# Performance work log

Hardware: AMD Instinct MI355X
Metric: run time of the kernel (lower is better)

Reference implementation:

```python
import jax, jax.numpy as jnp
from jax import lax
import numpy as np

_MAX_SQRT_GRADIENT = 1000.0

@jax.custom_vjp
def sqrt_bound_derivative(x):
    return jnp.sqrt(x)

def _sbd_fwd(x):
    return jnp.sqrt(x), x

def _sbd_bwd(x, g):
    clipped = jnp.clip(4.0 * x, 1.0 / _MAX_SQRT_GRADIENT**2)
    return (g / jnp.sqrt(clipped),)

sqrt_bound_derivative.defvjp(_sbd_fwd, _sbd_bwd)

HIDDEN = 2560
LRU = 2560
HEADS = 10
CONV_W = 4
BATCH = 2
SEQ = 4096


def setup_inputs() -> dict:
    key = jax.random.key(0)
    ks = jax.random.split(key, 12)
    s = 0.02  # init scale for weights
    inp = {
        'input_states': jax.random.normal(ks[0], (BATCH, SEQ, HIDDEN), jnp.float32),
        'position_ids': jnp.broadcast_to(jnp.arange(SEQ, dtype=jnp.int64), (BATCH, SEQ)),
        'prev_h': jnp.zeros((BATCH, LRU), jnp.float32),
        'w_y': jax.random.normal(ks[1], (LRU, HIDDEN), jnp.float32) * s,
        'b_y': jax.random.normal(ks[2], (LRU,), jnp.float32) * s,
        'w_x': jax.random.normal(ks[3], (LRU, HIDDEN), jnp.float32) * s,
        'b_x': jax.random.normal(ks[4], (LRU,), jnp.float32) * s,
        'w_out': jax.random.normal(ks[5], (HIDDEN, LRU), jnp.float32) * s,
        'b_out': jax.random.normal(ks[6], (HIDDEN,), jnp.float32) * s,
        'conv_w': jax.random.normal(ks[7], (LRU, CONV_W), jnp.float32) * 0.3,
        'conv_b': jax.random.normal(ks[8], (LRU,), jnp.float32) * s,
        'a_param': jax.random.normal(ks[9], (LRU,), jnp.float32),
        'ig_w': jax.random.normal(ks[10], (LRU // HEADS, LRU), jnp.float32) * s,
        'ig_b': jnp.zeros((LRU // HEADS,), jnp.float32),
        'ag_w': jax.random.normal(ks[11], (LRU // HEADS, LRU), jnp.float32) * s,
        'ag_b': jnp.zeros((LRU // HEADS,), jnp.float32),
    }
    return inp


def _block_gate(x_bshi, gate_w, gate_b, heads, bw):
    # gate_w is the nn.Linear weight [bw, heads*bw] reshaped to block-diagonal form
    w = gate_w.reshape(heads, bw, bw).transpose(0, 2, 1)  # h i j
    y = jnp.einsum('bshi,hij->bshj', x_bshi, w) + gate_b
    B, S = y.shape[0], y.shape[1]
    return jax.nn.sigmoid(y.reshape(B, S, heads * bw))


def _rglru(activations, position_ids, prev_h, a_param, ig_w, ig_b, ag_w, ag_b):
    B, S, D = activations.shape
    bw = ig_w.shape[0]
    heads = ig_w.shape[1] // bw
    reset = (position_ids[:, :, None] == 0)  # [B,S,1] bool
    x = activations.reshape(B, S, heads, bw)
    gate_x = _block_gate(x, ig_w, ig_b, heads, bw)  # [B,S,D]
    gate_a = _block_gate(x, ag_w, ag_b, heads, bw)  # [B,S,D]
    log_a = -8.0 * gate_a * jax.nn.softplus(a_param)
    a = jnp.exp(log_a)
    a_square = jnp.exp(2.0 * log_a)
    gated_x = activations * gate_x
    multiplier = sqrt_bound_derivative(1.0 - a_square)
    multiplier = jnp.where(reset, 1.0, multiplier)
    normalized_x = gated_x * multiplier.astype(activations.dtype)
    a = a * (~reset)  # zero the decay at document boundaries

    def step(h, inp):
        a_t, x_t = inp  # [B,D] each
        h = a_t.astype(jnp.float32) * h + x_t.astype(jnp.float32)
        return h, h.astype(activations.dtype)

    xs = (a.transpose(1, 0, 2), normalized_x.transpose(1, 0, 2))  # time-major
    last_h, y = lax.scan(step, prev_h, xs)
    return y.transpose(1, 0, 2), last_h


def reference(input_states, position_ids, prev_h, w_y, b_y, w_x, b_x,
              w_out, b_out, conv_w, conv_b, a_param, ig_w, ig_b, ag_w, ag_b):
    B, S, _ = input_states.shape
    # y branch: gelu(tanh approx)
    y_branch = jax.nn.gelu(input_states @ w_y.T + b_y, approximate=True)
    # x branch: linear + depthwise causal conv (kernel width CONV_W)
    x_branch = input_states @ w_x.T + b_x  # [B,S,LRU]
    Wd = conv_w.shape[1]
    xp = jnp.pad(x_branch, ((0, 0), (Wd - 1, 0), (0, 0)))
    conv_out = conv_b + sum(xp[:, k:k + S, :] * conv_w[:, k] for k in range(Wd))
    # RG-LRU
    h, last_h = _rglru(conv_out, position_ids, prev_h, a_param, ig_w, ig_b, ag_w, ag_b)
    h = h * y_branch
    out = h @ w_out.T + b_out
    return out
```

## Files before the change

### kernel.cpp

```cpp
#include <hip/hip_runtime.h>
#include <hip/hip_bf16.h>
#include <math.h>

typedef __hip_bfloat16 bf16;
typedef __attribute__((ext_vector_type(4))) float f32x4;
typedef __attribute__((ext_vector_type(8))) __bf16 bf16x8;

static constexpr int HID    = 2560;
static constexpr int LRUD   = 2560;
static constexpr int HEADSN = 10;
static constexpr int BWID   = 256;
static constexpr int SEQL   = 4096;
static constexpr int BATCHN = 2;
static constexpr int NTOK   = BATCHN * SEQL;
static constexpr int NCHUNK = 128;
static constexpr int CHLEN  = 32;

#define GAS __attribute__((address_space(1)))
#define LAS __attribute__((address_space(3)))
#define MEMFENCE asm volatile("" ::: "memory")
#define PHASE_SYNC                                        \
  __builtin_amdgcn_s_barrier(); MEMFENCE;                 \
  asm volatile("s_waitcnt lgkmcnt(0)" ::: "memory");
#define PHASE_END                                         \
  __builtin_amdgcn_s_barrier(); MEMFENCE;
#define VMGATE6 asm volatile("s_waitcnt vmcnt(6)" ::: "memory")
#define VMGATE0 asm volatile("s_waitcnt vmcnt(0)" ::: "memory")

__device__ __forceinline__ void async_copy16(void* lds, const void* g) {
  __builtin_amdgcn_global_load_lds((const GAS unsigned int*)g,
                                   (LAS unsigned int*)lds, 16, 0, 0);
}

__device__ __forceinline__ bf16x8 lds_frag(const bf16* tile, int row, int cb) {
  return *(const bf16x8*)((const char*)tile + row * 128 + (cb ^ ((row & 7) << 4)));
}

template<int EPI>
__global__ __launch_bounds__(512, 2)
void gemm256_kernel(const bf16* __restrict__ A, int lda,
                    const bf16* __restrict__ B0p, const bf16* __restrict__ B1p,
                    int ldb,
                    const float* __restrict__ bias0, const float* __restrict__ bias1,
                    void* __restrict__ out0, void* __restrict__ out1,
                    int ldc, int K)
{
  __shared__ __align__(16) bf16 As[2][256 * 64];
  __shared__ __align__(16) bf16 Bs[2][256 * 64];

  const int tid  = threadIdx.x;
  const int wave = tid >> 6;
  const int lane = tid & 63;
  const int wm   = wave >> 2;
  const int wn   = wave & 3;

  const int nxy  = gridDim.x * gridDim.y;
  const int orig = blockIdx.y * gridDim.x + blockIdx.x;
  const int swz  = (orig & 7) * (nxy >> 3) + (orig >> 3);
  const int m0   = (swz / gridDim.x) * 256;
  const int n0   = (swz % gridDim.x) * 256;

  const int zsel = (EPI == 1) ? (int)blockIdx.z : 0;
  const bf16*  Bw   = zsel ? B1p : B0p;
  const float* bias = zsel ? bias1 : bias0;

  const int NT = K / 64;
  f32x4  acc[8][4] = {};
  bf16x8 a[8], b[4][2];

  const int srow = tid >> 3;
  const int spb  = (tid & 7) * 16;

  auto stageA = [&](int t, int c) {
    const int r  = c * 64 + srow;
    const int cb = spb ^ ((r & 7) << 4);
    async_copy16(&As[t & 1][c * 4096 + wave * 512],
                 A + (size_t)(m0 + r) * lda + t * 64 + (cb >> 1));
  };
  auto stageB = [&](int t, int c) {
    const int r  = c * 64 + srow;
    const int cb = spb ^ ((r & 7) << 4);
    async_copy16(&Bs[t & 1][c * 4096 + wave * 512],
                 Bw + (size_t)(n0 + r) * ldb + t * 64 + (cb >> 1));
  };
  auto readA = [&](int buf, int ks) {
#pragma unroll
    for (int fm = 0; fm < 8; ++fm)
      a[fm] = lds_frag(As[buf], wm * 128 + fm * 16 + (lane & 15),
                       ks * 64 + (lane >> 4) * 16);
  };
  auto readB = [&](int buf) {
#pragma unroll
    for (int fn = 0; fn < 4; ++fn)
#pragma unroll
      for (int ks = 0; ks < 2; ++ks)
        b[fn][ks] = lds_frag(Bs[buf], wn * 64 + fn * 16 + (lane & 15),
                             ks * 64 + (lane >> 4) * 16);
  };
  auto mfma16 = [&](int ks, int fnb) {
#pragma unroll
    for (int fn = 0; fn < 4; ++fn) {
      if (fn != fnb && fn != fnb + 1) continue;
#pragma unroll
      for (int fm = 0; fm < 8; ++fm)
        acc[fm][fn] = __builtin_amdgcn_mfma_f32_16x16x32_bf16(a[fm], b[fn][ks],
                                                              acc[fm][fn], 0, 0, 0);
    }
  };

#pragma unroll
  for (int c = 0; c < 4; ++c) stageA(0, c);
#pragma unroll
  for (int c = 0; c < 4; ++c) stageB(0, c);
#pragma unroll
  for (int c = 0; c < 4; ++c) stageB(1, c);
  stageA(1, 0); stageA(1, 1);
  VMGATE6;
  PHASE_END;

  const int NI = NT / 2;
  for (int i = 0; i < NI; ++i) {
    const int  t0 = 2 * i, t1 = 2 * i + 1;
    const bool s2 = (t0 + 2) < NT;
    const bool s3 = (t1 + 2) < NT;

    readA(0, 0); readB(0);
    stageA(t1, 2); stageA(t1, 3);
    PHASE_SYNC;
    __builtin_amdgcn_s_setprio(1); mfma16(0, 0); __builtin_amdgcn_s_setprio(0);
    PHASE_END;
    if (s2) { stageB(t0 + 2, 0); stageB(t0 + 2, 1); }
    PHASE_SYNC;
    __builtin_amdgcn_s_setprio(1); mfma16(0, 2); __builtin_amdgcn_s_setprio(0);
    PHASE_END;
    readA(0, 1);
    if (s2) { stageB(t0 + 2, 2); stageB(t0 + 2, 3); }
    PHASE_SYNC;
    __builtin_amdgcn_s_setprio(1); mfma16(1, 0); __builtin_amdgcn_s_setprio(0);
    PHASE_END;
    if (s2) { stageA(t0 + 2, 0); stageA(t0 + 2, 1); }
    PHASE_SYNC;
    __builtin_amdgcn_s_setprio(1); mfma16(1, 2); __builtin_amdgcn_s_setprio(0);
    if (s2) { VMGATE6; } else { VMGATE0; }
    PHASE_END;
    readA(1, 0); readB(1);
    if (s2) { stageA(t0 + 2, 2); stageA(t0 + 2, 3); }
    PHASE_SYNC;
    __builtin_amdgcn_s_setprio(1); mfma16(0, 0); __builtin_amdgcn_s_setprio(0);
    PHASE_END;
    if (s3) { stageB(t1 + 2, 0); stageB(t1 + 2, 1); }
    PHASE_SYNC;
    __builtin_amdgcn_s_setprio(1); mfma16(0, 2); __builtin_amdgcn_s_setprio(0);
    PHASE_END;
    readA(1, 1);
    if (s3) { stageB(t1 + 2, 2); stageB(t1 + 2, 3); }
    PHASE_SYNC;
    __builtin_amdgcn_s_setprio(1); mfma16(1, 0); __builtin_amdgcn_s_setprio(0);
    PHASE_END;
    if (s3) { stageA(t1 + 2, 0); stageA(t1 + 2, 1); }
    PHASE_SYNC;
    __builtin_amdgcn_s_setprio(1); mfma16(1, 2); __builtin_amdgcn_s_setprio(0);
    if (s2) { if (s3) { VMGATE6; } else { VMGATE0; } }
    PHASE_END;
  }

  const int mrb = (lane >> 4) * 4;
  const int ncc = lane & 15;
#pragma unroll
  for (int fm = 0; fm < 8; ++fm) {
#pragma unroll
    for (int fn = 0; fn < 4; ++fn) {
      const int n  = n0 + wn * 64 + fn * 16 + ncc;
      const float bv = bias[n];
#pragma unroll
      for (int r = 0; r < 4; ++r) {
        const int m = m0 + wm * 128 + fm * 16 + mrb + r;
        const size_t idx = (size_t)m * ldc + n;
        float v = acc[fm][fn][r] + bv;
        if constexpr (EPI == 0) {
          ((float*)out0)[idx] = v;
        } else {
          if (zsel == 0) {
            const float t = tanhf(0.7978845608028654f * (v + 0.044715f * v * v * v));
            ((bf16*)out0)[idx] = __float2bfloat16(0.5f * v * (1.0f + t));
          } else {
            ((bf16*)out1)[idx] = __float2bfloat16(v);
          }
        }
      }
    }
  }
}

__global__ __launch_bounds__(256)
void gemm128_f32_kernel(const bf16* __restrict__ A, int lda,
                        const bf16* __restrict__ Bw, int ldb,
                        const float* __restrict__ bias,
                        float* __restrict__ C, int ldc, int K)
{
  __shared__ __align__(16) bf16 As[128 * 64];
  __shared__ __align__(16) bf16 Bs[128 * 64];

  const int tid  = threadIdx.x;
  const int wave = tid >> 6;
  const int lane = tid & 63;
  const int wy   = wave >> 1;
  const int wx   = wave & 1;
  const int m0   = blockIdx.y * 128;
  const int n0   = blockIdx.x * 128;

  f32x4 acc[4][4] = {};
  const int srow = tid >> 3;
  const int spb  = (tid & 7) * 16;

  for (int k0 = 0; k0 < K; k0 += 64) {
#pragma unroll
    for (int rd = 0; rd < 4; ++rd) {
      const int r  = rd * 32 + srow;
      const int cb = spb ^ ((r & 7) << 4);
      async_copy16(&As[rd * 2048 + wave * 512],
                   A + (size_t)(m0 + r) * lda + k0 + (cb >> 1));
      async_copy16(&Bs[rd * 2048 + wave * 512],
                   Bw + (size_t)(n0 + r) * ldb + k0 + (cb >> 1));
    }
    __syncthreads();
#pragma unroll
    for (int ks = 0; ks < 2; ++ks) {
      bf16x8 af[4], bfr[4];
      const int cb = ks * 64 + (lane >> 4) * 16;
#pragma unroll
      for (int f = 0; f < 4; ++f) {
        af[f]  = lds_frag(As, wy * 64 + f * 16 + (lane & 15), cb);
        bfr[f] = lds_frag(Bs, wx * 64 + f * 16 + (lane & 15), cb);
      }
#pragma unroll
      for (int fm = 0; fm < 4; ++fm)
#pragma unroll
        for (int fn = 0; fn < 4; ++fn)
          acc[fm][fn] = __builtin_amdgcn_mfma_f32_16x16x32_bf16(af[fm], bfr[fn], acc[fm][fn], 0, 0, 0);
    }
    __syncthreads();
  }

  const int mrb = (lane >> 4) * 4;
  const int ncc = lane & 15;
#pragma unroll
  for (int fm = 0; fm < 4; ++fm) {
#pragma unroll
    for (int fn = 0; fn < 4; ++fn) {
      const int n  = n0 + wx * 64 + fn * 16 + ncc;
      const float bv = bias[n];
#pragma unroll
      for (int r = 0; r < 4; ++r) {
        const int m = m0 + wy * 64 + fm * 16 + mrb + r;
        C[(size_t)m * ldc + n] = acc[fm][fn][r] + bv;
      }
    }
  }
}

__global__ __launch_bounds__(256)
void gate_gemm_kernel(const bf16* __restrict__ Conv,
                      const bf16* __restrict__ IGb, const bf16* __restrict__ AGb,
                      const float* __restrict__ ig_b, const float* __restrict__ ag_b,
                      bf16* __restrict__ Gx, bf16* __restrict__ Ga)
{
  __shared__ __align__(16) bf16 As[128 * 64];
  __shared__ __align__(16) bf16 Bs[128 * 64];

  const int tid  = threadIdx.x;
  const int wave = tid >> 6;
  const int lane = tid & 63;
  const int wy   = wave >> 1;
  const int wx   = wave & 1;
  const int m0   = blockIdx.y * 128;
  const int n0   = blockIdx.x * 128;
  const int head = blockIdx.z % HEADSN;
  const int sel  = blockIdx.z / HEADSN;

  const bf16*  A    = Conv + head * BWID;
  const bf16*  Bw   = (sel ? AGb : IGb) + (size_t)head * BWID * BWID;
  const float* bias = sel ? ag_b : ig_b;
  bf16*        Cp   = (sel ? Ga : Gx) + head * BWID;

  f32x4 acc[4][4] = {};
  const int srow = tid >> 3;
  const int spb  = (tid & 7) * 16;

  for (int k0 = 0; k0 < BWID; k0 += 64) {
#pragma unroll
    for (int rd = 0; rd < 4; ++rd) {
      const int r  = rd * 32 + srow;
      const int cb = spb ^ ((r & 7) << 4);
      async_copy16(&As[rd * 2048 + wave * 512],
                   A + (size_t)(m0 + r) * LRUD + k0 + (cb >> 1));
      async_copy16(&Bs[rd * 2048 + wave * 512],
                   Bw + (size_t)(n0 + r) * BWID + k0 + (cb >> 1));
    }
    __syncthreads();
#pragma unroll
    for (int ks = 0; ks < 2; ++ks) {
      bf16x8 af[4], bfr[4];
      const int cb = ks * 64 + (lane >> 4) * 16;
#pragma unroll
      for (int f = 0; f < 4; ++f) {
        af[f]  = lds_frag(As, wy * 64 + f * 16 + (lane & 15), cb);
        bfr[f] = lds_frag(Bs, wx * 64 + f * 16 + (lane & 15), cb);
      }
#pragma unroll
      for (int fm = 0; fm < 4; ++fm)
#pragma unroll
        for (int fn = 0; fn < 4; ++fn)
          acc[fm][fn] = __builtin_amdgcn_mfma_f32_16x16x32_bf16(af[fm], bfr[fn], acc[fm][fn], 0, 0, 0);
    }
    __syncthreads();
  }

  const int mrb = (lane >> 4) * 4;
  const int ncc = lane & 15;
#pragma unroll
  for (int fm = 0; fm < 4; ++fm) {
#pragma unroll
    for (int fn = 0; fn < 4; ++fn) {
      const int n  = n0 + wx * 64 + fn * 16 + ncc;
      const float bv = bias[n];
#pragma unroll
      for (int r = 0; r < 4; ++r) {
        const int m = m0 + wy * 64 + fm * 16 + mrb + r;
        float v = acc[fm][fn][r] + bv;
        Cp[(size_t)m * LRUD + n] = __float2bfloat16(1.0f / (1.0f + expf(-v)));
      }
    }
  }
}

static constexpr int CV0 = NTOK * HID / 4;
static constexpr int CVW = LRUD * HID / 4;
static constexpr int CVG = BWID * LRUD / 4;
static constexpr int CVT_TOTAL = CV0 + 3 * CVW + 2 * CVG;

__device__ __forceinline__ void cvt4(const float* src, bf16* dst, int j) {
  const float4 v = *(const float4*)(src + (size_t)j * 4);
  dst[(size_t)j * 4 + 0] = __float2bfloat16(v.x);
  dst[(size_t)j * 4 + 1] = __float2bfloat16(v.y);
  dst[(size_t)j * 4 + 2] = __float2bfloat16(v.z);
  dst[(size_t)j * 4 + 3] = __float2bfloat16(v.w);
}

__global__ __launch_bounds__(256)
void cvt_all_kernel(const float* __restrict__ x_in, const float* __restrict__ w_y,
                    const float* __restrict__ w_x, const float* __restrict__ w_out,
                    const float* __restrict__ ig_w, const float* __restrict__ ag_w,
                    bf16* __restrict__ Xbf, bf16* __restrict__ Wyb,
                    bf16* __restrict__ Wxb, bf16* __restrict__ Wob,
                    bf16* __restrict__ IGb, bf16* __restrict__ AGb)
{
  int g = blockIdx.x * 256 + threadIdx.x;
  if (g < CV0)                       { cvt4(x_in,  Xbf, g); return; }
  g -= CV0;
  if (g < CVW)                       { cvt4(w_y,   Wyb, g); return; }
  g -= CVW;
  if (g < CVW)                       { cvt4(w_x,   Wxb, g); return; }
  g -= CVW;
  if (g < CVW)                       { cvt4(w_out, Wob, g); return; }
  g -= CVW;
  if (g < CVG)                       { cvt4(ig_w,  IGb, g); return; }
  g -= CVG;
  cvt4(ag_w, AGb, g);
}

__global__ __launch_bounds__(256)
void conv_kernel(const bf16* __restrict__ Xb, const float* __restrict__ cw,
                 const float* __restrict__ cbias, bf16* __restrict__ out) {
  const int c  = blockIdx.x * 256 + threadIdx.x;
  const int t0 = blockIdx.y * 8;
  const int bb = blockIdx.z;
  size_t base = ((size_t)bb * SEQL + t0) * LRUD + c;
  const float w0 = cw[c * 4 + 0], w1 = cw[c * 4 + 1];
  const float w2 = cw[c * 4 + 2], w3 = cw[c * 4 + 3];
  const float bc = cbias[c];
  float xm1, xm2, xm3;
  if (blockIdx.y == 0) { xm1 = xm2 = xm3 = 0.f; }
  else {
    xm1 = __bfloat162float(Xb[base - (size_t)LRUD]);
    xm2 = __bfloat162float(Xb[base - (size_t)2 * LRUD]);
    xm3 = __bfloat162float(Xb[base - (size_t)3 * LRUD]);
  }
#pragma unroll
  for (int tl = 0; tl < 8; ++tl) {
    const float x = __bfloat162float(Xb[base]);
    out[base] = __float2bfloat16(bc + x * w3 + xm1 * w2 + xm2 * w1 + xm3 * w0);
    xm3 = xm2; xm2 = xm1; xm1 = x;
    base += LRUD;
  }
}

__device__ __forceinline__ void compute_ax(float conv, float gx, float ga, float sp,
                                           int t, float& a, float& x) {
  const float la  = -8.f * ga * sp;
  a               = expf(la);
  const float asq = expf(2.f * la);
  float mult      = sqrtf(fmaxf(1.f - asq, 0.f));
  if (t == 0) { a = 0.f; mult = 1.f; }
  x = conv * gx * mult;
}

__global__ __launch_bounds__(256)
void scan1_kernel(const bf16* __restrict__ conv, const bf16* __restrict__ gxb,
                  const bf16* __restrict__ gab, const float* __restrict__ a_param,
                  float* __restrict__ cA, float* __restrict__ cX) {
  const int c     = blockIdx.x * 256 + threadIdx.x;
  const int chunk = blockIdx.y;
  const int b     = blockIdx.z;
  const float ap  = a_param[c];
  const float sp  = (ap > 20.f) ? ap : log1pf(expf(ap));
  size_t base = ((size_t)b * SEQL + (size_t)chunk * CHLEN) * LRUD + c;
  float A = 1.f, X = 0.f;
  for (int tl = 0; tl < CHLEN; ++tl) {
    float a, x;
    compute_ax(__bfloat162float(conv[base]), __bfloat162float(gxb[base]),
               __bfloat162float(gab[base]), sp, chunk * CHLEN + tl, a, x);
    X = a * X + x;
    A *= a;
    base += LRUD;
  }
  const size_t ci = ((size_t)b * NCHUNK + chunk) * LRUD + c;
  cA[ci] = A;
  cX[ci] = X;
}

__global__ __launch_bounds__(256)
void scan2_kernel(const float* __restrict__ cA, const float* __restrict__ cX,
                  const float* __restrict__ prev_h, float* __restrict__ pref) {
  const int g = blockIdx.x * 256 + threadIdx.x;
  const int b = g / LRUD;
  const int c = g % LRUD;
  float h = prev_h[g];
#pragma unroll 8
  for (int ch = 0; ch < NCHUNK; ++ch) {
    const size_t ci = ((size_t)b * NCHUNK + ch) * LRUD + c;
    pref[ci] = h;
    h = cA[ci] * h + cX[ci];
  }
}

__global__ __launch_bounds__(256)
void scan3_kernel(const bf16* __restrict__ conv, const bf16* __restrict__ gxb,
                  const bf16* __restrict__ gab, const float* __restrict__ a_param,
                  const float* __restrict__ pref, const bf16* __restrict__ yb,
                  bf16* __restrict__ hm) {
  const int c     = blockIdx.x * 256 + threadIdx.x;
  const int chunk = blockIdx.y;
  const int b     = blockIdx.z;
  const float ap  = a_param[c];
  const float sp  = (ap > 20.f) ? ap : log1pf(expf(ap));
  float h = pref[((size_t)b * NCHUNK + chunk) * LRUD + c];
  size_t base = ((size_t)b * SEQL + (size_t)chunk * CHLEN) * LRUD + c;
  for (int tl = 0; tl < CHLEN; ++tl) {
    float a, x;
    compute_ax(__bfloat162float(conv[base]), __bfloat162float(gxb[base]),
               __bfloat162float(gab[base]), sp, chunk * CHLEN + tl, a, x);
    h = a * h + x;
    hm[base] = __float2bfloat16(h * __bfloat162float(yb[base]));
    base += LRUD;
  }
}

extern "C" void kernel_launch(void* const* d_in, const int* in_sizes, int n_in,
                              void* d_out, int out_size, void* d_ws, size_t ws_size,
                              hipStream_t stream) {
  const float* x_in    = (const float*)d_in[0];
  const float* prev_h  = (const float*)d_in[2];
  const float* w_y     = (const float*)d_in[3];
  const float* b_y     = (const float*)d_in[4];
  const float* w_x     = (const float*)d_in[5];
  const float* b_x     = (const float*)d_in[6];
  const float* w_out   = (const float*)d_in[7];
  const float* b_out   = (const float*)d_in[8];
  const float* conv_w  = (const float*)d_in[9];
  const float* conv_b  = (const float*)d_in[10];
  const float* a_param = (const float*)d_in[11];
  const float* ig_w    = (const float*)d_in[12];
  const float* ig_b    = (const float*)d_in[13];
  const float* ag_w    = (const float*)d_in[14];
  const float* ag_b    = (const float*)d_in[15];

  char* ws = (char*)d_ws;
  size_t off = 0;
  auto alloc = [&](size_t bytes) -> char* {
    char* p = ws + off;
    off += (bytes + 255) & ~(size_t)255;
    return p;
  };
  bf16*  Xbf  = (bf16*)alloc((size_t)NTOK * HID * 2);
  bf16*  Wyb  = (bf16*)alloc((size_t)LRUD * HID * 2);
  bf16*  Wxb  = (bf16*)alloc((size_t)LRUD * HID * 2);
  bf16*  Wob  = (bf16*)alloc((size_t)HID * LRUD * 2);
  bf16*  IGb  = (bf16*)alloc((size_t)BWID * LRUD * 2);
  bf16*  AGb  = (bf16*)alloc((size_t)BWID * LRUD * 2);
  bf16*  Conv = (bf16*)alloc((size_t)NTOK * LRUD * 2);
  float* cA   = (float*)alloc((size_t)BATCHN * NCHUNK * LRUD * 4);
  float* cX   = (float*)alloc((size_t)BATCHN * NCHUNK * LRUD * 4);
  float* pref = (float*)alloc((size_t)BATCHN * NCHUNK * LRUD * 4);

  bf16* Yb = (bf16*)d_out;
  bf16* Xb = (bf16*)d_out + (size_t)NTOK * LRUD;
  bf16* Gx = Xbf;
  bf16* Ga = Xb;
  bf16* Hm = Conv;

  cvt_all_kernel<<<dim3(CVT_TOTAL / 256), 256, 0, stream>>>(
      x_in, w_y, w_x, w_out, ig_w, ag_w, Xbf, Wyb, Wxb, Wob, IGb, AGb);

  gemm256_kernel<1><<<dim3(LRUD / 256, NTOK / 256, 2), 512, 0, stream>>>(
      Xbf, HID, Wyb, Wxb, HID, b_y, b_x, Yb, Xb, LRUD, HID);
  conv_kernel<<<dim3(LRUD / 256, SEQL / 8, BATCHN), 256, 0, stream>>>(
      Xb, conv_w, conv_b, Conv);
  gate_gemm_kernel<<<dim3(BWID / 128, NTOK / 128, 2 * HEADSN), 256, 0, stream>>>(
      Conv, IGb, AGb, ig_b, ag_b, Gx, Ga);
  scan1_kernel<<<dim3(LRUD / 256, NCHUNK, BATCHN), 256, 0, stream>>>(
      Conv, Gx, Ga, a_param, cA, cX);
  scan2_kernel<<<dim3((BATCHN * LRUD) / 256), 256, 0, stream>>>(cA, cX, prev_h, pref);
  scan3_kernel<<<dim3(LRUD / 256, NCHUNK, BATCHN), 256, 0, stream>>>(
      Conv, Gx, Ga, a_param, pref, Yb, Hm);
  gemm128_f32_kernel<<<dim3(HID / 128, NTOK / 128), 256, 0, stream>>>(
      Hm, LRUD, Wob, LRUD, b_out, (float*)d_out, HID, LRUD);

  (void)in_sizes; (void)n_in; (void)out_size; (void)ws_size;
}
```

Baseline: 575.4 us.

## Make dual input GEMM persistent with 128x256 tiles over 256 blocks

Result: slower. 600.7 us (+4.4%).

```diff
diff --git a/kernel.cpp b/kernel.cpp
--- a/kernel.cpp
+++ b/kernel.cpp
@@ -36,16 +36,13 @@
   return *(const bf16x8*)((const char*)tile + row * 128 + (cb ^ ((row & 7) << 4)));
 }
 
-template<int EPI>
 __global__ __launch_bounds__(512, 2)
-void gemm256_kernel(const bf16* __restrict__ A, int lda,
-                    const bf16* __restrict__ B0p, const bf16* __restrict__ B1p,
-                    int ldb,
-                    const float* __restrict__ bias0, const float* __restrict__ bias1,
-                    void* __restrict__ out0, void* __restrict__ out1,
-                    int ldc, int K)
+void dual_persist_kernel(const bf16* __restrict__ A,
+                         const bf16* __restrict__ B0p, const bf16* __restrict__ B1p,
+                         const float* __restrict__ bias0, const float* __restrict__ bias1,
+                         bf16* __restrict__ out0, bf16* __restrict__ out1)
 {
-  __shared__ __align__(16) bf16 As[2][256 * 64];
+  __shared__ __align__(16) bf16 As[2][128 * 64];
   __shared__ __align__(16) bf16 Bs[2][256 * 64];
 
   const int tid  = threadIdx.x;
@@ -53,138 +50,129 @@
   const int lane = tid & 63;
   const int wm   = wave >> 2;
   const int wn   = wave & 3;
-
-  const int nxy  = gridDim.x * gridDim.y;
-  const int orig = blockIdx.y * gridDim.x + blockIdx.x;
-  const int swz  = (orig & 7) * (nxy >> 3) + (orig >> 3);
-  const int m0   = (swz / gridDim.x) * 256;
-  const int n0   = (swz % gridDim.x) * 256;
-
-  const int zsel = (EPI == 1) ? (int)blockIdx.z : 0;
-  const bf16*  Bw   = zsel ? B1p : B0p;
-  const float* bias = zsel ? bias1 : bias0;
-
-  const int NT = K / 64;
-  f32x4  acc[8][4] = {};
-  bf16x8 a[8], b[4][2];
-
   const int srow = tid >> 3;
   const int spb  = (tid & 7) * 16;
-
-  auto stageA = [&](int t, int c) {
-    const int r  = c * 64 + srow;
-    const int cb = spb ^ ((r & 7) << 4);
-    async_copy16(&As[t & 1][c * 4096 + wave * 512],
-                 A + (size_t)(m0 + r) * lda + t * 64 + (cb >> 1));
-  };
-  auto stageB = [&](int t, int c) {
-    const int r  = c * 64 + srow;
-    const int cb = spb ^ ((r & 7) << 4);
-    async_copy16(&Bs[t & 1][c * 4096 + wave * 512],
-                 Bw + (size_t)(n0 + r) * ldb + t * 64 + (cb >> 1));
-  };
-  auto readA = [&](int buf, int ks) {
-#pragma unroll
-    for (int fm = 0; fm < 8; ++fm)
-      a[fm] = lds_frag(As[buf], wm * 128 + fm * 16 + (lane & 15),
-                       ks * 64 + (lane >> 4) * 16);
-  };
-  auto readB = [&](int buf) {
-#pragma unroll
-    for (int fn = 0; fn < 4; ++fn)
-#pragma unroll
-      for (int ks = 0; ks < 2; ++ks)
-        b[fn][ks] = lds_frag(Bs[buf], wn * 64 + fn * 16 + (lane & 15),
-                             ks * 64 + (lane >> 4) * 16);
-  };
-  auto mfma16 = [&](int ks, int fnb) {
-#pragma unroll
-    for (int fn = 0; fn < 4; ++fn) {
-      if (fn != fnb && fn != fnb + 1) continue;
-#pragma unroll
-      for (int fm = 0; fm < 8; ++fm)
-        acc[fm][fn] = __builtin_amdgcn_mfma_f32_16x16x32_bf16(a[fm], b[fn][ks],
-                                                              acc[fm][fn], 0, 0, 0);
-    }
-  };
-
-#pragma unroll
-  for (int c = 0; c < 4; ++c) stageA(0, c);
-#pragma unroll
-  for (int c = 0; c < 4; ++c) stageB(0, c);
-#pragma unroll
-  for (int c = 0; c < 4; ++c) stageB(1, c);
-  stageA(1, 0); stageA(1, 1);
-  VMGATE6;
-  PHASE_END;
-
-  const int NI = NT / 2;
-  for (int i = 0; i < NI; ++i) {
-    const int  t0 = 2 * i, t1 = 2 * i + 1;
-    const bool s2 = (t0 + 2) < NT;
-    const bool s3 = (t1 + 2) < NT;
-
-    readA(0, 0); readB(0);
-    stageA(t1, 2); stageA(t1, 3);
-    PHASE_SYNC;
-    __builtin_amdgcn_s_setprio(1); mfma16(0, 0); __builtin_amdgcn_s_setprio(0);
-    PHASE_END;
-    if (s2) { stageB(t0 + 2, 0); stageB(t0 + 2, 1); }
-    PHASE_SYNC;
-    __builtin_amdgcn_s_setprio(1); mfma16(0, 2); __builtin_amdgcn_s_setprio(0);
-    PHASE_END;
-    readA(0, 1);
-    if (s2) { stageB(t0 + 2, 2); stageB(t0 + 2, 3); }
-    PHASE_SYNC;
-    __builtin_amdgcn_s_setprio(1); mfma16(1, 0); __builtin_amdgcn_s_setprio(0);
-    PHASE_END;
-    if (s2) { stageA(t0 + 2, 0); stageA(t0 + 2, 1); }
-    PHASE_SYNC;
-    __builtin_amdgcn_s_setprio(1); mfma16(1, 2); __builtin_amdgcn_s_setprio(0);
-    if (s2) { VMGATE6; } else { VMGATE0; }
-    PHASE_END;
-    readA(1, 0); readB(1);
-    if (s2) { stageA(t0 + 2, 2); stageA(t0 + 2, 3); }
-    PHASE_SYNC;
-    __builtin_amdgcn_s_setprio(1); mfma16(0, 0); __builtin_amdgcn_s_setprio(0);
-    PHASE_END;
-    if (s3) { stageB(t1 + 2, 0); stageB(t1 + 2, 1); }
-    PHASE_SYNC;
-    __builtin_amdgcn_s_setprio(1); mfma16(0, 2); __builtin_amdgcn_s_setprio(0);
-    PHASE_END;
-    readA(1, 1);
-    if (s3) { stageB(t1 + 2, 2); stageB(t1 + 2, 3); }
-    PHASE_SYNC;
-    __builtin_amdgcn_s_setprio(1); mfma16(1, 0); __builtin_amdgcn_s_setprio(0);
-    PHASE_END;
-    if (s3) { stageA(t1 + 2, 0); stageA(t1 + 2, 1); }
-    PHASE_SYNC;
-    __builtin_amdgcn_s_setprio(1); mfma16(1, 2); __builtin_amdgcn_s_setprio(0);
-    if (s2) { if (s3) { VMGATE6; } else { VMGATE0; } }
-    PHASE_END;
-  }
-
+  static constexpr int NT = HID / 64;
   const int mrb = (lane >> 4) * 4;
   const int ncc = lane & 15;
-#pragma unroll
-  for (int fm = 0; fm < 8; ++fm) {
-#pragma unroll
-    for (int fn = 0; fn < 4; ++fn) {
-      const int n  = n0 + wn * 64 + fn * 16 + ncc;
-      const float bv = bias[n];
-#pragma unroll
-      for (int r = 0; r < 4; ++r) {
-        const int m = m0 + wm * 128 + fm * 16 + mrb + r;
-        const size_t idx = (size_t)m * ldc + n;
-        float v = acc[fm][fn][r] + bv;
-        if constexpr (EPI == 0) {
-          ((float*)out0)[idx] = v;
-        } else {
-          if (zsel == 0) {
+
+  for (int j = 0; j < 5; ++j) {
+    const int s   = blockIdx.x * 5 + j;
+    const int z   = s / 640;
+    const int r   = s % 640;
+    const int n0  = (r / 64) * 256;
+    const int m0  = (r % 64) * 128;
+    const bf16*  Bw   = z ? B1p : B0p;
+    const float* bias = z ? bias1 : bias0;
+    bf16*        outp = z ? out1 : out0;
+
+    f32x4  acc[4][4] = {};
+    bf16x8 a[4], b[4][2];
+
+    auto stageA = [&](int t, int c) {
+      const int rr = c * 64 + srow;
+      const int cb = spb ^ ((rr & 7) << 4);
+      async_copy16(&As[t & 1][c * 4096 + wave * 512],
+                   A + (size_t)(m0 + rr) * HID + t * 64 + (cb >> 1));
+    };
+    auto stageB = [&](int t, int c) {
+      const int rr = c * 64 + srow;
+      const int cb = spb ^ ((rr & 7) << 4);
+      async_copy16(&Bs[t & 1][c * 4096 + wave * 512],
+                   Bw + (size_t)(n0 + rr) * HID + t * 64 + (cb >> 1));
+    };
+    auto readA = [&](int buf, int ks) {
+#pragma unroll
+      for (int fm = 0; fm < 4; ++fm)
+        a[fm] = lds_frag(As[buf], wm * 64 + fm * 16 + (lane & 15),
+                         ks * 64 + (lane >> 4) * 16);
+    };
+    auto readB = [&](int buf) {
+#pragma unroll
+      for (int fn = 0; fn < 4; ++fn)
+#pragma unroll
+        for (int ks = 0; ks < 2; ++ks)
+          b[fn][ks] = lds_frag(Bs[buf], wn * 64 + fn * 16 + (lane & 15),
+                               ks * 64 + (lane >> 4) * 16);
+    };
+    auto mfma8 = [&](int ks, int fnb) {
+#pragma unroll
+      for (int fn = 0; fn < 4; ++fn) {
+        if (fn != fnb && fn != fnb + 1) continue;
+#pragma unroll
+        for (int fm = 0; fm < 4; ++fm)
+          acc[fm][fn] = __builtin_amdgcn_mfma_f32_16x16x32_bf16(a[fm], b[fn][ks],
+                                                                acc[fm][fn], 0, 0, 0);
+      }
+    };
+
+#pragma unroll
+    for (int c = 0; c < 4; ++c) stageB(0, c);
+    stageA(0, 0); stageA(0, 1);
+#pragma unroll
+    for (int c = 0; c < 4; ++c) stageB(1, c);
+    stageA(1, 0); stageA(1, 1);
+    VMGATE6;
+    PHASE_END;
+
+    for (int i = 0; i < NT / 2; ++i) {
+      const int  t0 = 2 * i, t1 = 2 * i + 1;
+      const bool s2 = (t0 + 2) < NT;
+      const bool s3 = (t1 + 2) < NT;
+
+      readA(0, 0); readB(0);
+      PHASE_SYNC;
+      __builtin_amdgcn_s_setprio(1); mfma8(0, 0); __builtin_amdgcn_s_setprio(0);
+      PHASE_END;
+      if (s2) { stageB(t0 + 2, 0); stageB(t0 + 2, 1); }
+      PHASE_SYNC;
+      __builtin_amdgcn_s_setprio(1); mfma8(0, 2); __builtin_amdgcn_s_setprio(0);
+      PHASE_END;
+      readA(0, 1);
+      if (s2) { stageB(t0 + 2, 2); stageB(t0 + 2, 3); }
+      PHASE_SYNC;
+      __builtin_amdgcn_s_setprio(1); mfma8(1, 0); __builtin_amdgcn_s_setprio(0);
+      PHASE_END;
+      if (s2) { stageA(t0 + 2, 0); stageA(t0 + 2, 1); }
+      PHASE_SYNC;
+      __builtin_amdgcn_s_setprio(1); mfma8(1, 2); __builtin_amdgcn_s_setprio(0);
+      if (s2) { VMGATE6; } else { VMGATE0; }
+      PHASE_END;
+      readA(1, 0); readB(1);
+      PHASE_SYNC;
+      __builtin_amdgcn_s_setprio(1); mfma8(0, 0); __builtin_amdgcn_s_setprio(0);
+      PHASE_END;
+      if (s3) { stageB(t1 + 2, 0); stageB(t1 + 2, 1); }
+      PHASE_SYNC;
+      __builtin_amdgcn_s_setprio(1); mfma8(0, 2); __builtin_amdgcn_s_setprio(0);
+      PHASE_END;
+      readA(1, 1);
+      if (s3) { stageB(t1 + 2, 2); stageB(t1 + 2, 3); }
+      PHASE_SYNC;
+      __builtin_amdgcn_s_setprio(1); mfma8(1, 0); __builtin_amdgcn_s_setprio(0);
+      PHASE_END;
+      if (s3) { stageA(t1 + 2, 0); stageA(t1 + 2, 1); }
+      PHASE_SYNC;
+      __builtin_amdgcn_s_setprio(1); mfma8(1, 2); __builtin_amdgcn_s_setprio(0);
+      if (s2) { if (s3) { VMGATE6; } else { VMGATE0; } }
+      PHASE_END;
+    }
+
+#pragma unroll
+    for (int fm = 0; fm < 4; ++fm) {
+#pragma unroll
+      for (int fn = 0; fn < 4; ++fn) {
+        const int n  = n0 + wn * 64 + fn * 16 + ncc;
+        const float bv = bias[n];
+#pragma unroll
+        for (int rr = 0; rr < 4; ++rr) {
+          const int m = m0 + wm * 64 + fm * 16 + mrb + rr;
+          float v = acc[fm][fn][rr] + bv;
+          if (z == 0) {
             const float t = tanhf(0.7978845608028654f * (v + 0.044715f * v * v * v));
-            ((bf16*)out0)[idx] = __float2bfloat16(0.5f * v * (1.0f + t));
+            outp[(size_t)m * LRUD + n] = __float2bfloat16(0.5f * v * (1.0f + t));
           } else {
-            ((bf16*)out1)[idx] = __float2bfloat16(v);
+            outp[(size_t)m * LRUD + n] = __float2bfloat16(v);
           }
         }
       }
@@ -512,8 +500,8 @@
   cvt_all_kernel<<<dim3(CVT_TOTAL / 256), 256, 0, stream>>>(
       x_in, w_y, w_x, w_out, ig_w, ag_w, Xbf, Wyb, Wxb, Wob, IGb, AGb);
 
-  gemm256_kernel<1><<<dim3(LRUD / 256, NTOK / 256, 2), 512, 0, stream>>>(
-      Xbf, HID, Wyb, Wxb, HID, b_y, b_x, Yb, Xb, LRUD, HID);
+  dual_persist_kernel<<<dim3(256), 512, 0, stream>>>(
+      Xbf, Wyb, Wxb, b_y, b_x, Yb, Xb);
   conv_kernel<<<dim3(LRUD / 256, SEQL / 8, BATCHN), 256, 0, stream>>>(
       Xb, conv_w, conv_b, Conv);
   gate_gemm_kernel<<<dim3(BWID / 128, NTOK / 128, 2 * HEADSN), 256, 0, stream>>>(
```
